# Kernel tuning notes

Measured on AMD Instinct MI355X. Metric: run time of the kernel, lower is better.

The kernel has to match this reference:

```python
import jax, jax.numpy as jnp
import numpy as np
import math

N = 50000        # nodes
DEG = 16         # regular out-degree -> E = N*DEG edges, grouped by source node
B = 64           # graphs in batch
F = 128          # num_node_features
H = 128          # nhid == enhid
RATIO = 0.5      # edge_ratio
NUM_CONVS = 3
E = N * DEG


def setup_inputs() -> dict:
    key = jax.random.key(0)
    ks = jax.random.split(key, 18)
    s = 0.05
    x = jax.random.normal(ks[0], (N, F), jnp.float32)
    edge_src = jnp.repeat(jnp.arange(N, dtype=jnp.int32), DEG)          # sorted by src
    edge_dst = jax.random.randint(ks[1], (E,), 0, N, jnp.int32)
    batch = ((jnp.arange(N) * B) // N).astype(jnp.int32)                 # sorted graph ids
    edge_attr = jnp.ones((E, 1), jnp.float32)                            # edge_attr=None branch
    inp = {"x": x, "edge_attr": edge_attr, "edge_src": edge_src,
           "edge_dst": edge_dst, "batch": batch}
    # GCNConv weights: [F->H, H->H, H->H]
    inp["W_gcn0"] = jax.random.normal(ks[2], (F, H), jnp.float32) * s
    inp["b_gcn0"] = jnp.zeros((H,), jnp.float32)
    inp["W_gcn1"] = jax.random.normal(ks[3], (H, H), jnp.float32) * s
    inp["b_gcn1"] = jnp.zeros((H,), jnp.float32)
    inp["W_gcn2"] = jax.random.normal(ks[4], (H, H), jnp.float32) * s
    inp["b_gcn2"] = jnp.zeros((H,), jnp.float32)
    # EGNN edge convs: [1->H, H->H]
    inp["W_eg0"] = jax.random.normal(ks[5], (1, H), jnp.float32) * s
    inp["b_eg0"] = jnp.zeros((H,), jnp.float32)
    inp["W_eg1"] = jax.random.normal(ks[6], (H, H), jnp.float32) * s
    inp["b_eg1"] = jnp.zeros((H,), jnp.float32)
    # score convs: [H->1, H->1]
    inp["W_sc0"] = jax.random.normal(ks[7], (H, 1), jnp.float32) * s
    inp["b_sc0"] = jnp.zeros((1,), jnp.float32)
    inp["W_sc1"] = jax.random.normal(ks[8], (H, 1), jnp.float32) * s
    inp["b_sc1"] = jnp.zeros((1,), jnp.float32)
    return inp


def _gcn(x, src, dst, ew, W, b):
    # PyG GCNConv: add self-loops (weight 1), symmetric deg normalization, aggregate at dst.
    n = x.shape[0]
    loop = jnp.arange(n, dtype=src.dtype)
    src2 = jnp.concatenate([src, loop])
    dst2 = jnp.concatenate([dst, loop])
    ew2 = jnp.concatenate([ew, jnp.ones((n,), ew.dtype)])
    deg = jax.ops.segment_sum(ew2, dst2, n)
    dinv = jnp.where(deg > 0, jax.lax.rsqrt(jnp.maximum(deg, 1e-12)), 0.0)
    norm = dinv[src2] * dinv[dst2] * ew2                                  # [E+n]
    msg = (x @ W)[src2] * norm[:, None]                                    # gather + scale
    return jax.ops.segment_sum(msg, dst2, n) + b                           # scatter-add


def _egnn(e, src, W, b):
    # Edge conv: scatter edge features to their source node, gather back, linear map.
    agg = jax.ops.segment_sum(e, src, N)
    return agg[src] @ W + b


def _pool(h, batch):
    gmax = jax.ops.segment_max(h, batch, B)
    gsum = jax.ops.segment_sum(h, batch, B)
    cnt = jax.ops.segment_sum(jnp.ones((h.shape[0],), h.dtype), batch, B)
    gmean = gsum / cnt[:, None]
    return jnp.concatenate([gmax, gmean, gsum], axis=1)                    # [B, 3H]


def reference(x, edge_attr, edge_src, edge_dst, batch,
              W_gcn0, b_gcn0, W_gcn1, b_gcn1, W_gcn2, b_gcn2,
              W_eg0, b_eg0, W_eg1, b_eg1, W_sc0, b_sc0, W_sc1, b_sc1):
    gW = [W_gcn0, W_gcn1, W_gcn2]
    gb = [b_gcn0, b_gcn1, b_gcn2]
    eW = [W_eg0, W_eg1]
    eb = [b_eg0, b_eg1]
    sW = [W_sc0, W_sc1]
    sb = [b_sc0, b_sc1]
    src, dst = edge_src, edge_dst
    deg = DEG
    ew = jnp.ones((src.shape[0],), jnp.float32)
    h = x
    ea = edge_attr
    xs = jnp.zeros((B, 3 * H), jnp.float32)
    for i in range(NUM_CONVS):
        h = jax.nn.relu(_gcn(h, src, dst, ew, gW[i], gb[i]))
        if i < NUM_CONVS - 1:
            ea = jax.nn.relu(_egnn(ea, src, eW[i], eb[i]))
            score = jnp.tanh(_egnn(ea, src, sW[i], sb[i])[:, 0])           # [E_cur]
            k = math.ceil(RATIO * deg)                                      # per-src-node top-k
            vals, idx = jax.lax.top_k(score.reshape(N, deg), k)             # [N,k]
            dst = jnp.take_along_axis(dst.reshape(N, deg), idx, axis=1).reshape(-1)
            flat = (jnp.arange(N)[:, None] * deg + idx).reshape(-1)
            ea = ea[flat]
            src = jnp.repeat(jnp.arange(N, dtype=src.dtype), k)
            ew = jnp.clip(vals.reshape(-1), 0.0, 1.0)
            deg = k
        xs = xs + _pool(h, batch)
    return xs
```

## Files before the change

### kernel.cpp

```cpp
#include <hip/hip_runtime.h>
#include <math.h>

#define NNODES 50000
#define DEGREE 16
#define NGRAPH 64
#define CAP 64
#define LDA 136
#define NXCD 8
#define XRANGE (NNODES / NXCD)
#define NTILE 782
#define ACHUNK 784
#define BCAP 192

typedef unsigned short u16;
typedef unsigned int u32;
typedef unsigned long long u64;
using short8 = __attribute__((ext_vector_type(8))) short;
using f32x4  = __attribute__((ext_vector_type(4))) float;
using fv4    = __attribute__((ext_vector_type(4))) float;
using u16x4  = __attribute__((ext_vector_type(4))) unsigned short;

__device__ __forceinline__ u16 f2bf(float f) {
  union { float f; u32 u; } v; v.f = f;
  u32 u = v.u;
  return (u16)((u + 0x7FFFu + ((u >> 16) & 1u)) >> 16);
}
__device__ __forceinline__ float2 bf2x2(u32 u) {
  union { u32 u; float f; } lo, hi;
  lo.u = (u & 0xFFFFu) << 16; hi.u = u & 0xFFFF0000u;
  return make_float2(lo.f, hi.f);
}
__device__ __forceinline__ u32 pack2(float x, float y) {
  return (u32)f2bf(x) | ((u32)f2bf(y) << 16);
}
__device__ __forceinline__ int lowerb(const int* b, int n, int v) {
  int lo = 0, hi = n;
  while (lo < hi) { int m = (lo + hi) >> 1; if (b[m] < v) lo = m + 1; else hi = m; }
  return lo;
}

__device__ __forceinline__ void cons8(uint4 v, float w, float* acc) {
  float2 p;
  p = bf2x2(v.x); acc[0] = fmaf(w, p.x, acc[0]); acc[1] = fmaf(w, p.y, acc[1]);
  p = bf2x2(v.y); acc[2] = fmaf(w, p.x, acc[2]); acc[3] = fmaf(w, p.y, acc[3]);
  p = bf2x2(v.z); acc[4] = fmaf(w, p.x, acc[4]); acc[5] = fmaf(w, p.y, acc[5]);
  p = bf2x2(v.w); acc[6] = fmaf(w, p.x, acc[6]); acc[7] = fmaf(w, p.y, acc[7]);
}
__device__ __forceinline__ void consP(uint4 v, float* mx, float* sm) {
  float2 p;
  p = bf2x2(v.x);
  mx[0] = fmaxf(mx[0], p.x); sm[0] += p.x; mx[1] = fmaxf(mx[1], p.y); sm[1] += p.y;
  p = bf2x2(v.y);
  mx[2] = fmaxf(mx[2], p.x); sm[2] += p.x; mx[3] = fmaxf(mx[3], p.y); sm[3] += p.y;
  p = bf2x2(v.z);
  mx[4] = fmaxf(mx[4], p.x); sm[4] += p.x; mx[5] = fmaxf(mx[5], p.y); sm[5] += p.y;
  p = bf2x2(v.w);
  mx[6] = fmaxf(mx[6], p.x); sm[6] += p.x; mx[7] = fmaxf(mx[7], p.y); sm[7] += p.y;
}

__global__ __launch_bounds__(256) void k_init(
    const float* __restrict__ eattr, const float* __restrict__ x,
    const float* __restrict__ weg, const float* __restrict__ beg,
    const float* __restrict__ wsc, const float* __restrict__ bsc,
    const float* __restrict__ W0, const float* __restrict__ W1,
    const float* __restrict__ W2, const float* __restrict__ W3,
    float* __restrict__ ew1, float* __restrict__ agg0,
    u16* __restrict__ xb, u16* __restrict__ Wt,
    const int* __restrict__ edst, int* __restrict__ cnt,
    int* __restrict__ slots, int2* __restrict__ stag, int* __restrict__ scnt) {
  __shared__ int2 lbuf[NXCD * BCAP];
  __shared__ int lcnt[NXCD];
  int b = blockIdx.x, t = threadIdx.x;
  if (b < 6250) {
    int i = b * 256 + t;
    fv4 v = __builtin_nontemporal_load(&reinterpret_cast<const fv4*>(x)[i]);
    u16x4 o = {f2bf(v.x), f2bf(v.y), f2bf(v.z), f2bf(v.w)};
    reinterpret_cast<u16x4*>(xb)[i] = o;
    if (i < NNODES) {
      const fv4* p = reinterpret_cast<const fv4*>(eattr + (size_t)i * DEGREE);
      float s = 0.f;
#pragma unroll
      for (int j = 0; j < 4; ++j) {
        fv4 w = __builtin_nontemporal_load(&p[j]);
        s += w.x + w.y + w.z + w.w;
      }
      agg0[i] = s;
      float sc = 0.f;
      for (int k = 0; k < 128; ++k) {
        float e = fmaxf(fmaf(s, weg[k], beg[k]), 0.f);
        sc = fmaf(e, wsc[k], sc);
      }
      float v1 = tanhf(fmaf(16.f, sc, bsc[0]));
      ew1[i] = fminf(fmaxf(v1, 0.f), 1.f);
    }
  } else if (b < 6506) {
    int idx = (b - 6250) * 256 + t;
    int which = idx >> 14, r = idx & 16383;
    int k = r >> 7, n = r & 127;
    const float* W = which == 0 ? W0 : which == 1 ? W1 : which == 2 ? W2 : W3;
    Wt[which * 16384 + n * 128 + k] = f2bf(W[k * 128 + n]);
  } else {
    int b2 = b - 6506;
    if (t < NXCD) lcnt[t] = 0;
    __syncthreads();
    int e0 = b2 * ACHUNK;
    for (int k = 0; k < ACHUNK; k += 256) {
      int idx = k + t;
      int e = e0 + idx;
      if (idx < ACHUNK && e < NNODES * DEGREE) {
        int d = edst[e];
        u32 r = (u32)d / (u32)XRANGE;
        int pos = atomicAdd(&lcnt[r], 1);
        if (pos < BCAP) {
          lbuf[r * BCAP + pos] = make_int2(e, d);
        } else {
          int gp = atomicAdd(&cnt[d], 1);
          if (gp < CAP) slots[(size_t)d * CAP + gp] = e;
        }
      }
    }
    __syncthreads();
    for (int idx = t; idx < NXCD * BCAP; idx += 256) {
      int r = idx / BCAP, i = idx - r * BCAP;
      if (i < min(lcnt[r], BCAP))
        stag[((size_t)r * 1024 + b2) * BCAP + i] = lbuf[idx];
    }
    if (t < NXCD) scnt[t * 1024 + b2] = min(lcnt[t], BCAP);
  }
}

__global__ __launch_bounds__(256) void k_fillB(
    const int2* __restrict__ stag, const int* __restrict__ scnt,
    int* __restrict__ cnt, int* __restrict__ slots) {
  int kk = blockIdx.x;
  int r = kk & (NXCD - 1), sub = kk >> 3;
  for (int q = 0; q < 8; ++q) {
    int sb = sub * 8 + q;
    int c = scnt[r * 1024 + sb];
    const int2* src = &stag[((size_t)r * 1024 + sb) * BCAP];
    for (int i = threadIdx.x; i < c; i += 256) {
      int2 v = src[i];
      int pos = atomicAdd(&cnt[v.y], 1);
      if (pos < CAP) slots[(size_t)v.y * CAP + pos] = v.x;
    }
  }
}

__global__ __launch_bounds__(256) void k_gemmF(
    int nGemm, const u16* __restrict__ A, const u16* __restrict__ WtA,
    u16* __restrict__ outA,
    int nEg, const float* __restrict__ agg0, const float* __restrict__ weg,
    const float* __restrict__ beg, const u16* __restrict__ WtE,
    const float* __restrict__ beE, const float* __restrict__ wsc1,
    const float* __restrict__ bs1, float* __restrict__ ewOut) {
  __shared__ u16 Bs[128 * LDA];
  __shared__ u16 As[64 * LDA];
  int b = blockIdx.x, t = threadIdx.x;
  int eg = (b >= nGemm);
  const u16* Wsrc = eg ? WtE : WtA;
  for (int i = t; i < 2048; i += 256) {
    int r = i >> 4, c = (i & 15) << 3;
    *reinterpret_cast<uint4*>(&Bs[r * LDA + c]) =
        *reinterpret_cast<const uint4*>(&Wsrc[r * 128 + c]);
  }
  int m0 = (eg ? (b - nGemm) : b) * 64;
  if (eg) {
    for (int idx = t; idx < 64 * 128; idx += 256) {
      int r = idx >> 7, k = idx & 127;
      int row = m0 + r;
      float a = (row < NNODES) ? agg0[row] : 0.f;
      float v = 8.f * fmaxf(fmaf(a, weg[k], beg[k]), 0.f);
      As[r * LDA + k] = f2bf(v);
    }
  } else {
    for (int i = t; i < 1024; i += 256) {
      int r = i >> 4, c = (i & 15) << 3;
      int row = m0 + r;
      uint4 v = make_uint4(0u, 0u, 0u, 0u);
      if (row < NNODES) v = *reinterpret_cast<const uint4*>(&A[(size_t)row * 128 + c]);
      *reinterpret_cast<uint4*>(&As[r * LDA + c]) = v;
    }
  }
  __syncthreads();
  int wave = t >> 6, lane = t & 63;
  int lm = lane & 15, quad = lane >> 4;
  f32x4 z = {0.f, 0.f, 0.f, 0.f};
  f32x4 acc[8];
#pragma unroll
  for (int n = 0; n < 8; ++n) acc[n] = z;
  const u16* arow = &As[(wave * 16 + lm) * LDA + quad * 8];
#pragma unroll
  for (int kc = 0; kc < 4; ++kc) {
    short8 af = *reinterpret_cast<const short8*>(arow + kc * 32);
#pragma unroll
    for (int n = 0; n < 8; ++n) {
      short8 bf = *reinterpret_cast<const short8*>(
          &Bs[(n * 16 + lm) * LDA + kc * 32 + quad * 8]);
      acc[n] = __builtin_amdgcn_mfma_f32_16x16x32_bf16(af, bf, acc[n], 0, 0, 0);
    }
  }
  if (!eg) {
#pragma unroll
    for (int n = 0; n < 8; ++n) {
      int col = n * 16 + lm;
#pragma unroll
      for (int r = 0; r < 4; ++r) {
        int row = m0 + wave * 16 + quad * 4 + r;
        if (row < NNODES) outA[(size_t)row * 128 + col] = f2bf(acc[n][r]);
      }
    }
  } else {
    float s0 = 0.f, s1 = 0.f, s2 = 0.f, s3 = 0.f;
#pragma unroll
    for (int n = 0; n < 8; ++n) {
      int col = n * 16 + lm;
      float bb = beE[col], wv = wsc1[col];
      s0 = fmaf(fmaxf(acc[n][0] + bb, 0.f), wv, s0);
      s1 = fmaf(fmaxf(acc[n][1] + bb, 0.f), wv, s1);
      s2 = fmaf(fmaxf(acc[n][2] + bb, 0.f), wv, s2);
      s3 = fmaf(fmaxf(acc[n][3] + bb, 0.f), wv, s3);
    }
#pragma unroll
    for (int m = 8; m >= 1; m >>= 1) {
      s0 += __shfl_xor(s0, m, 64);
      s1 += __shfl_xor(s1, m, 64);
      s2 += __shfl_xor(s2, m, 64);
      s3 += __shfl_xor(s3, m, 64);
    }
    if (lm == 0) {
      float bsv = bs1[0];
      float sv[4] = {s0, s1, s2, s3};
#pragma unroll
      for (int r = 0; r < 4; ++r) {
        int row = m0 + wave * 16 + quad * 4 + r;
        if (row < NNODES) {
          float v = tanhf(fmaf(8.f, sv[r], bsv));
          ewOut[row] = fminf(fmaxf(v, 0.f), 1.f);
        }
      }
    }
  }
}

__global__ __launch_bounds__(256) void k_aggp(
    int nAgg, const u16* __restrict__ xwb, const int* __restrict__ cnt,
    const int* __restrict__ slots, const float* __restrict__ wsrc,
    const float* __restrict__ dinv, const float* __restrict__ bias,
    u16* __restrict__ hout, int keep, int l0mode,
    const u16* __restrict__ hpool, const int* __restrict__ batch,
    float* __restrict__ out, int poolAdd,
    const float* __restrict__ ew1g, float* __restrict__ dv1,
    float* __restrict__ ws1,
    const float* __restrict__ ew2g, float* __restrict__ dv2,
    float* __restrict__ ws2) {
  __shared__ float P[1024];
  int b = blockIdx.x, t = threadIdx.x;
  int lane = t & 63;
  int q = lane >> 4, li = lane & 15;
  if (b < nAgg) {
    int n = (b * 256 + t) >> 6;
    if (n >= NNODES) return;
    int c = min(cnt[n], CAP);
    u32 e = 0;
    if (lane < c) e = (u32)slots[(size_t)n * CAP + lane];
    if (l0mode) {
      u32 j = e & 15u; int srcn = (int)(e >> 4);
      float e1 = 0.f, e2 = 0.f;
      if (lane < c && j < 8u) {
        e1 = ew1g[srcn];
        if (j < 4u) e2 = ew2g[srcn];
      }
#pragma unroll
      for (int m = 32; m >= 1; m >>= 1) {
        e1 += __shfl_xor(e1, m, 64);
        e2 += __shfl_xor(e2, m, 64);
      }
      if (lane == 0) {
        float d1 = rsqrtf(1.0f + e1), d2 = rsqrtf(1.0f + e2);
        dv1[n] = d1; ws1[n] = d1 * ew1g[n];
        dv2[n] = d2; ws2[n] = d2 * ew2g[n];
      }
    }
    int kc; u32 ce;
    if (keep < 16) {
      bool valid = (lane < c) && ((e & 15u) < (u32)keep);
      u64 mask = __ballot(valid);
      kc = (int)__popcll(mask);
      u64 lt = ((u64)1 << lane) - 1;
      int pos = valid ? (int)__popcll(mask & lt) : 63 - (int)__popcll((~mask) & lt);
      ce = (u32)__builtin_amdgcn_ds_permute(pos << 2, (int)e);
    } else { kc = c; ce = e; }
    int sl = 0; float wl = 0.f;
    if (lane < kc) {
      sl = (int)(ce >> 4);
      wl = l0mode ? rsqrtf(1.0f + (float)min(cnt[sl], CAP)) : wsrc[sl];
    }
    const uint4* b4 = reinterpret_cast<const uint4*>(xwb);
    uint4 selfv = b4[n * 16 + li];
    float acc[8] = {0.f, 0.f, 0.f, 0.f, 0.f, 0.f, 0.f, 0.f};
    for (int i = 0; i < kc; i += 16) {
      int r0 = i + q, r1 = i + 4 + q, r2 = i + 8 + q, r3 = i + 12 + q;
      int s0 = __shfl(sl, r0, 64); float w0 = __shfl(wl, r0, 64);
      int s1 = __shfl(sl, r1, 64); float w1 = __shfl(wl, r1, 64);
      int s2 = __shfl(sl, r2, 64); float w2 = __shfl(wl, r2, 64);
      int s3 = __shfl(sl, r3, 64); float w3 = __shfl(wl, r3, 64);
      if (r0 >= kc) { s0 = n; w0 = 0.f; }
      if (r1 >= kc) { s1 = n; w1 = 0.f; }
      if (r2 >= kc) { s2 = n; w2 = 0.f; }
      if (r3 >= kc) { s3 = n; w3 = 0.f; }
      uint4 v0 = b4[s0 * 16 + li];
      uint4 v1 = selfv, v2 = selfv, v3 = selfv;
      if (i + 4 < kc)  v1 = b4[s1 * 16 + li];
      if (i + 8 < kc)  v2 = b4[s2 * 16 + li];
      if (i + 12 < kc) v3 = b4[s3 * 16 + li];
      cons8(v0, w0, acc);
      cons8(v1, w1, acc);
      cons8(v2, w2, acc);
      cons8(v3, w3, acc);
    }
#pragma unroll
    for (int k = 0; k < 8; ++k) {
      acc[k] += __shfl_xor(acc[k], 16, 64);
      acc[k] += __shfl_xor(acc[k], 32, 64);
    }
    float di = l0mode ? rsqrtf(1.0f + (float)c) : dinv[n];
    float dd = di * di;
    const f32x4* bp = reinterpret_cast<const f32x4*>(bias);
    f32x4 bv0 = bp[li * 2], bv1 = bp[li * 2 + 1];
    float2 p0 = bf2x2(selfv.x), p1 = bf2x2(selfv.y),
           p2 = bf2x2(selfv.z), p3 = bf2x2(selfv.w);
    float r0 = fmaxf(fmaf(di, acc[0], fmaf(dd, p0.x, bv0.x)), 0.f);
    float r1 = fmaxf(fmaf(di, acc[1], fmaf(dd, p0.y, bv0.y)), 0.f);
    float r2 = fmaxf(fmaf(di, acc[2], fmaf(dd, p1.x, bv0.z)), 0.f);
    float r3 = fmaxf(fmaf(di, acc[3], fmaf(dd, p1.y, bv0.w)), 0.f);
    float r4 = fmaxf(fmaf(di, acc[4], fmaf(dd, p2.x, bv1.x)), 0.f);
    float r5 = fmaxf(fmaf(di, acc[5], fmaf(dd, p2.y, bv1.y)), 0.f);
    float r6 = fmaxf(fmaf(di, acc[6], fmaf(dd, p3.x, bv1.z)), 0.f);
    float r7 = fmaxf(fmaf(di, acc[7], fmaf(dd, p3.y, bv1.w)), 0.f);
    if (q == 0) {
      uint4 o;
      o.x = pack2(r0, r1); o.y = pack2(r2, r3);
      o.z = pack2(r4, r5); o.w = pack2(r6, r7);
      reinterpret_cast<uint4*>(hout + (size_t)n * 128)[li] = o;
    }
  } else {
    int g = b - nAgg;
    int wv = t >> 6;
    int lo = lowerb(batch, NNODES, g);
    int hi = lowerb(batch, NNODES, g + 1);
    const uint4* hb4 = reinterpret_cast<const uint4*>(hpool);
    float mx[8] = {0.f, 0.f, 0.f, 0.f, 0.f, 0.f, 0.f, 0.f};
    float sm[8] = {0.f, 0.f, 0.f, 0.f, 0.f, 0.f, 0.f, 0.f};
    int n = lo + wv * 4 + q;
    for (; n + 48 < hi; n += 64) {
      uint4 v0 = hb4[(size_t)n * 16 + li];
      uint4 v1 = hb4[(size_t)(n + 16) * 16 + li];
      uint4 v2 = hb4[(size_t)(n + 32) * 16 + li];
      uint4 v3 = hb4[(size_t)(n + 48) * 16 + li];
      consP(v0, mx, sm); consP(v1, mx, sm);
      consP(v2, mx, sm); consP(v3, mx, sm);
    }
    for (; n < hi; n += 16) {
      uint4 v = hb4[(size_t)n * 16 + li];
      consP(v, mx, sm);
    }
#pragma unroll
    for (int k = 0; k < 8; ++k) {
      mx[k] = fmaxf(mx[k], __shfl_xor(mx[k], 16, 64));
      mx[k] = fmaxf(mx[k], __shfl_xor(mx[k], 32, 64));
      sm[k] += __shfl_xor(sm[k], 16, 64);
      sm[k] += __shfl_xor(sm[k], 32, 64);
    }
    if (q == 0) {
#pragma unroll
      for (int k = 0; k < 8; ++k) {
        P[(wv * 16 + li) * 16 + k] = mx[k];
        P[(wv * 16 + li) * 16 + 8 + k] = sm[k];
      }
    }
    __syncthreads();
    if (t < 128) {
      int li2 = t >> 3, k = t & 7;
      int o0 = li2 * 16 + k, o1 = o0 + 8;
      float m = fmaxf(fmaxf(P[o0], P[256 + o0]),
                      fmaxf(P[512 + o0], P[768 + o0]));
      float s = P[o1] + P[256 + o1] + P[512 + o1] + P[768 + o1];
      float cf = (float)(hi - lo);
      int col = li2 * 8 + k;
      float* og = out + g * 384;
      if (poolAdd) {
        og[col] += m; og[128 + col] += s / cf; og[256 + col] += s;
      } else {
        og[col] = m;  og[128 + col] = s / cf;  og[256 + col] = s;
      }
    }
  }
}

extern "C" void kernel_launch(void* const* d_in, const int* in_sizes, int n_in,
                              void* d_out, int out_size, void* d_ws, size_t ws_size,
                              hipStream_t stream) {
  const float* x     = (const float*)d_in[0];
  const float* eattr = (const float*)d_in[1];
  const int*   edst  = (const int*)d_in[3];
  const int*   batch = (const int*)d_in[4];
  const float* Wg0 = (const float*)d_in[5];  const float* bg0 = (const float*)d_in[6];
  const float* Wg1 = (const float*)d_in[7];  const float* bg1 = (const float*)d_in[8];
  const float* Wg2 = (const float*)d_in[9];  const float* bg2 = (const float*)d_in[10];
  const float* We0 = (const float*)d_in[11]; const float* be0 = (const float*)d_in[12];
  const float* We1 = (const float*)d_in[13]; const float* be1 = (const float*)d_in[14];
  const float* Ws0 = (const float*)d_in[15]; const float* bs0 = (const float*)d_in[16];
  const float* Ws1 = (const float*)d_in[17]; const float* bs1 = (const float*)d_in[18];
  float* out = (float*)d_out;

  char* ws = (char*)d_ws;
  const size_t NBH = (size_t)NNODES * 128 * 2;
  size_t off = 0;
  auto alloc = [&](size_t bytes) { void* p = ws + off; off = (off + bytes + 255) & ~(size_t)255; return p; };
  u16*   Xb    = (u16*)alloc(NBH);
  u16*   XWb   = (u16*)alloc(NBH);
  u16*   Hb0   = (u16*)alloc(NBH);
  u16*   Hb1   = (u16*)alloc(NBH);
  u16*   Hb2   = (u16*)alloc(NBH);
  u16*   Wtb   = (u16*)alloc(4 * 128 * 128 * 2);
  int*   slots = (int*)alloc((size_t)NNODES * CAP * 4);
  int*   cnt   = (int*)alloc((size_t)NNODES * 4);
  int2*  stag  = (int2*)alloc((size_t)NXCD * 1024 * BCAP * 8);
  int*   scnt  = (int*)alloc((size_t)NXCD * 1024 * 4);
  float* agg0  = (float*)alloc((size_t)NNODES * 4);
  float* ew1   = (float*)alloc((size_t)NNODES * 4);
  float* ew2   = (float*)alloc((size_t)NNODES * 4);
  float* dinv1 = (float*)alloc((size_t)NNODES * 4);
  float* wsrc1 = (float*)alloc((size_t)NNODES * 4);
  float* dinv2 = (float*)alloc((size_t)NNODES * 4);
  float* wsrc2 = (float*)alloc((size_t)NNODES * 4);

  hipMemsetAsync(cnt, 0, (size_t)NNODES * 4, stream);
  k_init<<<7530, 256, 0, stream>>>(eattr, x, We0, be0, Ws0, bs0,
                                   Wg0, Wg1, Wg2, We1, ew1, agg0, Xb, Wtb,
                                   edst, cnt, slots, stag, scnt);
  k_fillB<<<1024, 256, 0, stream>>>(stag, scnt, cnt, slots);
  k_gemmF<<<2 * NTILE, 256, 0, stream>>>(
      NTILE, Xb, Wtb, XWb,
      NTILE, agg0, We0, be0, Wtb + 3 * 16384, be1, Ws1, bs1, ew2);
  k_aggp<<<12500, 256, 0, stream>>>(12500, XWb, cnt, slots, nullptr, nullptr, bg0,
                                    Hb0, 16, 1, nullptr, batch, nullptr, 0,
                                    ew1, dinv1, wsrc1, ew2, dinv2, wsrc2);
  k_gemmF<<<NTILE, 256, 0, stream>>>(
      NTILE, Hb0, Wtb + 16384, XWb,
      0, nullptr, nullptr, nullptr, nullptr, nullptr, nullptr, nullptr, nullptr);
  k_aggp<<<12500 + NGRAPH, 256, 0, stream>>>(12500, XWb, cnt, slots, wsrc1, dinv1,
                                             bg1, Hb1, 8, 0, Hb0, batch, out, 0,
                                             nullptr, nullptr, nullptr,
                                             nullptr, nullptr, nullptr);
  k_gemmF<<<NTILE, 256, 0, stream>>>(
      NTILE, Hb1, Wtb + 2 * 16384, XWb,
      0, nullptr, nullptr, nullptr, nullptr, nullptr, nullptr, nullptr, nullptr);
  k_aggp<<<12500 + NGRAPH, 256, 0, stream>>>(12500, XWb, cnt, slots, wsrc2, dinv2,
                                             bg2, Hb2, 4, 0, Hb1, batch, out, 1,
                                             nullptr, nullptr, nullptr,
                                             nullptr, nullptr, nullptr);
  k_aggp<<<NGRAPH, 256, 0, stream>>>(0, nullptr, cnt, slots, nullptr, nullptr,
                                     nullptr, nullptr, 0, 0, Hb2, batch, out, 1,
                                     nullptr, nullptr, nullptr,
                                     nullptr, nullptr, nullptr);
}
```

Measured before the change: 327.9 us.

## Fuse x bf16 conversion into first GEMM, merge fill kernel, templatize aggregation

The separate pass that converts x to bf16 in k_init is dropped. The first GEMM now loads fp32 x directly and packs it to bf16 while filling shared memory, which avoids writing and re-reading a bf16 copy of x. The k_fillB bucket-fill work is folded into the first k_gemmF launch as extra leading blocks, removing one kernel launch. k_aggp becomes a template on MODE so keep, layer-0 mode and pool-add are compile-time constants. The risk is that fill blocks and GEMM blocks now share one launch, and the GEMM reads twice as many bytes per A tile.

```diff
diff --git a/kernel.cpp b/kernel.cpp
--- a/kernel.cpp
+++ b/kernel.cpp
@@ -18,7 +18,6 @@
 using short8 = __attribute__((ext_vector_type(8))) short;
 using f32x4  = __attribute__((ext_vector_type(4))) float;
 using fv4    = __attribute__((ext_vector_type(4))) float;
-using u16x4  = __attribute__((ext_vector_type(4))) unsigned short;
 
 __device__ __forceinline__ u16 f2bf(float f) {
   union { float f; u32 u; } v; v.f = f;
@@ -59,23 +58,19 @@
 }
 
 __global__ __launch_bounds__(256) void k_init(
-    const float* __restrict__ eattr, const float* __restrict__ x,
+    const float* __restrict__ eattr,
     const float* __restrict__ weg, const float* __restrict__ beg,
     const float* __restrict__ wsc, const float* __restrict__ bsc,
     const float* __restrict__ W0, const float* __restrict__ W1,
     const float* __restrict__ W2, const float* __restrict__ W3,
-    float* __restrict__ ew1, float* __restrict__ agg0,
-    u16* __restrict__ xb, u16* __restrict__ Wt,
+    float* __restrict__ ew1, float* __restrict__ agg0, u16* __restrict__ Wt,
     const int* __restrict__ edst, int* __restrict__ cnt,
     int* __restrict__ slots, int2* __restrict__ stag, int* __restrict__ scnt) {
   __shared__ int2 lbuf[NXCD * BCAP];
   __shared__ int lcnt[NXCD];
   int b = blockIdx.x, t = threadIdx.x;
-  if (b < 6250) {
+  if (b < 196) {
     int i = b * 256 + t;
-    fv4 v = __builtin_nontemporal_load(&reinterpret_cast<const fv4*>(x)[i]);
-    u16x4 o = {f2bf(v.x), f2bf(v.y), f2bf(v.z), f2bf(v.w)};
-    reinterpret_cast<u16x4*>(xb)[i] = o;
     if (i < NNODES) {
       const fv4* p = reinterpret_cast<const fv4*>(eattr + (size_t)i * DEGREE);
       float s = 0.f;
@@ -93,14 +88,14 @@
       float v1 = tanhf(fmaf(16.f, sc, bsc[0]));
       ew1[i] = fminf(fmaxf(v1, 0.f), 1.f);
     }
-  } else if (b < 6506) {
-    int idx = (b - 6250) * 256 + t;
+  } else if (b < 452) {
+    int idx = (b - 196) * 256 + t;
     int which = idx >> 14, r = idx & 16383;
     int k = r >> 7, n = r & 127;
     const float* W = which == 0 ? W0 : which == 1 ? W1 : which == 2 ? W2 : W3;
     Wt[which * 16384 + n * 128 + k] = f2bf(W[k * 128 + n]);
   } else {
-    int b2 = b - 6506;
+    int b2 = b - 452;
     if (t < NXCD) lcnt[t] = 0;
     __syncthreads();
     int e0 = b2 * ACHUNK;
@@ -129,26 +124,11 @@
   }
 }
 
-__global__ __launch_bounds__(256) void k_fillB(
-    const int2* __restrict__ stag, const int* __restrict__ scnt,
-    int* __restrict__ cnt, int* __restrict__ slots) {
-  int kk = blockIdx.x;
-  int r = kk & (NXCD - 1), sub = kk >> 3;
-  for (int q = 0; q < 8; ++q) {
-    int sb = sub * 8 + q;
-    int c = scnt[r * 1024 + sb];
-    const int2* src = &stag[((size_t)r * 1024 + sb) * BCAP];
-    for (int i = threadIdx.x; i < c; i += 256) {
-      int2 v = src[i];
-      int pos = atomicAdd(&cnt[v.y], 1);
-      if (pos < CAP) slots[(size_t)v.y * CAP + pos] = v.x;
-    }
-  }
-}
-
 __global__ __launch_bounds__(256) void k_gemmF(
-    int nGemm, const u16* __restrict__ A, const u16* __restrict__ WtA,
-    u16* __restrict__ outA,
+    int nFill, const int2* __restrict__ stag, const int* __restrict__ scnt,
+    int* __restrict__ cnt, int* __restrict__ slots,
+    int nGemm, const u16* __restrict__ A, const float* __restrict__ Af32,
+    const u16* __restrict__ WtA, u16* __restrict__ outA,
     int nEg, const float* __restrict__ agg0, const float* __restrict__ weg,
     const float* __restrict__ beg, const u16* __restrict__ WtE,
     const float* __restrict__ beE, const float* __restrict__ wsc1,
@@ -156,14 +136,29 @@
   __shared__ u16 Bs[128 * LDA];
   __shared__ u16 As[64 * LDA];
   int b = blockIdx.x, t = threadIdx.x;
-  int eg = (b >= nGemm);
+  if (b < nFill) {
+    int r = b & (NXCD - 1), sub = b >> 3;
+    for (int q = 0; q < 8; ++q) {
+      int sb = sub * 8 + q;
+      int c = scnt[r * 1024 + sb];
+      const int2* src = &stag[((size_t)r * 1024 + sb) * BCAP];
+      for (int i = t; i < c; i += 256) {
+        int2 v = src[i];
+        int pos = atomicAdd(&cnt[v.y], 1);
+        if (pos < CAP) slots[(size_t)v.y * CAP + pos] = v.x;
+      }
+    }
+    return;
+  }
+  int bb = b - nFill;
+  int eg = (bb >= nGemm);
   const u16* Wsrc = eg ? WtE : WtA;
   for (int i = t; i < 2048; i += 256) {
     int r = i >> 4, c = (i & 15) << 3;
     *reinterpret_cast<uint4*>(&Bs[r * LDA + c]) =
         *reinterpret_cast<const uint4*>(&Wsrc[r * 128 + c]);
   }
-  int m0 = (eg ? (b - nGemm) : b) * 64;
+  int m0 = (eg ? (bb - nGemm) : bb) * 64;
   if (eg) {
     for (int idx = t; idx < 64 * 128; idx += 256) {
       int r = idx >> 7, k = idx & 127;
@@ -172,6 +167,20 @@
       float v = 8.f * fmaxf(fmaf(a, weg[k], beg[k]), 0.f);
       As[r * LDA + k] = f2bf(v);
     }
+  } else if (Af32) {
+    for (int i = t; i < 1024; i += 256) {
+      int r = i >> 4, c = (i & 15) << 3;
+      int row = m0 + r;
+      uint4 o = make_uint4(0u, 0u, 0u, 0u);
+      if (row < NNODES) {
+        const fv4* px = reinterpret_cast<const fv4*>(Af32 + (size_t)row * 128 + c);
+        fv4 v0 = __builtin_nontemporal_load(&px[0]);
+        fv4 v1 = __builtin_nontemporal_load(&px[1]);
+        o.x = pack2(v0.x, v0.y); o.y = pack2(v0.z, v0.w);
+        o.z = pack2(v1.x, v1.y); o.w = pack2(v1.z, v1.w);
+      }
+      *reinterpret_cast<uint4*>(&As[r * LDA + c]) = o;
+    }
   } else {
     for (int i = t; i < 1024; i += 256) {
       int r = i >> 4, c = (i & 15) << 3;
@@ -214,11 +223,11 @@
 #pragma unroll
     for (int n = 0; n < 8; ++n) {
       int col = n * 16 + lm;
-      float bb = beE[col], wv = wsc1[col];
-      s0 = fmaf(fmaxf(acc[n][0] + bb, 0.f), wv, s0);
-      s1 = fmaf(fmaxf(acc[n][1] + bb, 0.f), wv, s1);
-      s2 = fmaf(fmaxf(acc[n][2] + bb, 0.f), wv, s2);
-      s3 = fmaf(fmaxf(acc[n][3] + bb, 0.f), wv, s3);
+      float bb2 = beE[col], wv = wsc1[col];
+      s0 = fmaf(fmaxf(acc[n][0] + bb2, 0.f), wv, s0);
+      s1 = fmaf(fmaxf(acc[n][1] + bb2, 0.f), wv, s1);
+      s2 = fmaf(fmaxf(acc[n][2] + bb2, 0.f), wv, s2);
+      s3 = fmaf(fmaxf(acc[n][3] + bb2, 0.f), wv, s3);
     }
 #pragma unroll
     for (int m = 8; m >= 1; m >>= 1) {
@@ -242,17 +251,21 @@
   }
 }
 
-__global__ __launch_bounds__(256) void k_aggp(
+template <int MODE>
+__global__ __launch_bounds__(256) void k_agg(
     int nAgg, const u16* __restrict__ xwb, const int* __restrict__ cnt,
     const int* __restrict__ slots, const float* __restrict__ wsrc,
     const float* __restrict__ dinv, const float* __restrict__ bias,
-    u16* __restrict__ hout, int keep, int l0mode,
+    u16* __restrict__ hout,
     const u16* __restrict__ hpool, const int* __restrict__ batch,
-    float* __restrict__ out, int poolAdd,
+    float* __restrict__ out,
     const float* __restrict__ ew1g, float* __restrict__ dv1,
     float* __restrict__ ws1,
     const float* __restrict__ ew2g, float* __restrict__ dv2,
     float* __restrict__ ws2) {
+  constexpr int keep = (MODE == 0) ? 16 : (MODE == 1) ? 8 : 4;
+  constexpr bool L0 = (MODE == 0);
+  constexpr int poolAdd = (MODE >= 2);
   __shared__ float P[1024];
   int b = blockIdx.x, t = threadIdx.x;
   int lane = t & 63;
@@ -263,7 +276,7 @@
     int c = min(cnt[n], CAP);
     u32 e = 0;
     if (lane < c) e = (u32)slots[(size_t)n * CAP + lane];
-    if (l0mode) {
+    if (L0) {
       u32 j = e & 15u; int srcn = (int)(e >> 4);
       float e1 = 0.f, e2 = 0.f;
       if (lane < c && j < 8u) {
@@ -293,7 +306,7 @@
     int sl = 0; float wl = 0.f;
     if (lane < kc) {
       sl = (int)(ce >> 4);
-      wl = l0mode ? rsqrtf(1.0f + (float)min(cnt[sl], CAP)) : wsrc[sl];
+      wl = L0 ? rsqrtf(1.0f + (float)min(cnt[sl], CAP)) : wsrc[sl];
     }
     const uint4* b4 = reinterpret_cast<const uint4*>(xwb);
     uint4 selfv = b4[n * 16 + li];
@@ -323,7 +336,7 @@
       acc[k] += __shfl_xor(acc[k], 16, 64);
       acc[k] += __shfl_xor(acc[k], 32, 64);
     }
-    float di = l0mode ? rsqrtf(1.0f + (float)c) : dinv[n];
+    float di = L0 ? rsqrtf(1.0f + (float)c) : dinv[n];
     float dd = di * di;
     const f32x4* bp = reinterpret_cast<const f32x4*>(bias);
     f32x4 bv0 = bp[li * 2], bv1 = bp[li * 2 + 1];
@@ -417,7 +430,6 @@
   const size_t NBH = (size_t)NNODES * 128 * 2;
   size_t off = 0;
   auto alloc = [&](size_t bytes) { void* p = ws + off; off = (off + bytes + 255) & ~(size_t)255; return p; };
-  u16*   Xb    = (u16*)alloc(NBH);
   u16*   XWb   = (u16*)alloc(NBH);
   u16*   Hb0   = (u16*)alloc(NBH);
   u16*   Hb1   = (u16*)alloc(NBH);
@@ -436,32 +448,34 @@
   float* wsrc2 = (float*)alloc((size_t)NNODES * 4);
 
   hipMemsetAsync(cnt, 0, (size_t)NNODES * 4, stream);
-  k_init<<<7530, 256, 0, stream>>>(eattr, x, We0, be0, Ws0, bs0,
-                                   Wg0, Wg1, Wg2, We1, ew1, agg0, Xb, Wtb,
+  k_init<<<1476, 256, 0, stream>>>(eattr, We0, be0, Ws0, bs0,
+                                   Wg0, Wg1, Wg2, We1, ew1, agg0, Wtb,
                                    edst, cnt, slots, stag, scnt);
-  k_fillB<<<1024, 256, 0, stream>>>(stag, scnt, cnt, slots);
-  k_gemmF<<<2 * NTILE, 256, 0, stream>>>(
-      NTILE, Xb, Wtb, XWb,
+  k_gemmF<<<1024 + 2 * NTILE, 256, 0, stream>>>(
+      1024, stag, scnt, cnt, slots,
+      NTILE, nullptr, x, Wtb, XWb,
       NTILE, agg0, We0, be0, Wtb + 3 * 16384, be1, Ws1, bs1, ew2);
-  k_aggp<<<12500, 256, 0, stream>>>(12500, XWb, cnt, slots, nullptr, nullptr, bg0,
-                                    Hb0, 16, 1, nullptr, batch, nullptr, 0,
-                                    ew1, dinv1, wsrc1, ew2, dinv2, wsrc2);
+  k_agg<0><<<12500, 256, 0, stream>>>(12500, XWb, cnt, slots, nullptr, nullptr,
+                                      bg0, Hb0, nullptr, batch, nullptr,
+                                      ew1, dinv1, wsrc1, ew2, dinv2, wsrc2);
   k_gemmF<<<NTILE, 256, 0, stream>>>(
-      NTILE, Hb0, Wtb + 16384, XWb,
+      0, nullptr, nullptr, nullptr, nullptr,
+      NTILE, Hb0, nullptr, Wtb + 16384, XWb,
       0, nullptr, nullptr, nullptr, nullptr, nullptr, nullptr, nullptr, nullptr);
-  k_aggp<<<12500 + NGRAPH, 256, 0, stream>>>(12500, XWb, cnt, slots, wsrc1, dinv1,
-                                             bg1, Hb1, 8, 0, Hb0, batch, out, 0,
-                                             nullptr, nullptr, nullptr,
-                                             nullptr, nullptr, nullptr);
+  k_agg<1><<<12500 + NGRAPH, 256, 0, stream>>>(12500, XWb, cnt, slots, wsrc1,
+                                               dinv1, bg1, Hb1, Hb0, batch, out,
+                                               nullptr, nullptr, nullptr,
+                                               nullptr, nullptr, nullptr);
   k_gemmF<<<NTILE, 256, 0, stream>>>(
-      NTILE, Hb1, Wtb + 2 * 16384, XWb,
+      0, nullptr, nullptr, nullptr, nullptr,
+      NTILE, Hb1, nullptr, Wtb + 2 * 16384, XWb,
       0, nullptr, nullptr, nullptr, nullptr, nullptr, nullptr, nullptr, nullptr);
-  k_aggp<<<12500 + NGRAPH, 256, 0, stream>>>(12500, XWb, cnt, slots, wsrc2, dinv2,
-                                             bg2, Hb2, 4, 0, Hb1, batch, out, 1,
-                                             nullptr, nullptr, nullptr,
-                                             nullptr, nullptr, nullptr);
-  k_aggp<<<NGRAPH, 256, 0, stream>>>(0, nullptr, cnt, slots, nullptr, nullptr,
-                                     nullptr, nullptr, 0, 0, Hb2, batch, out, 1,
-                                     nullptr, nullptr, nullptr,
-                                     nullptr, nullptr, nullptr);
-}
+  k_agg<2><<<12500 + NGRAPH, 256, 0, stream>>>(12500, XWb, cnt, slots, wsrc2,
+                                               dinv2, bg2, Hb2, Hb1, batch, out,
+                                               nullptr, nullptr, nullptr,
+                                               nullptr, nullptr, nullptr);
+  k_agg<3><<<NGRAPH, 256, 0, stream>>>(0, nullptr, cnt, slots, nullptr, nullptr,
+                                       nullptr, nullptr, Hb2, batch, out,
+                                       nullptr, nullptr, nullptr,
+                                       nullptr, nullptr, nullptr);
+}
```

New measurement: 319.6 us. 1.03x faster.
